# Optimization experiments

Hardware: AMD Instinct MI355X
Metric: run time of the kernel (lower is better)

## Reference

```python
import jax, jax.numpy as jnp
import numpy as np

SR = 44100        # sample rate (init kwarg)
WINDOWS = 2048    # fft window size (init kwarg)
B, P = 128, 192   # batch, number of peaking filters


def setup_inputs() -> dict:
    key = jax.random.key(0)
    k1, k2, k3 = jax.random.split(key, 3)
    # center frequencies in (40 Hz, 0.45*sr), gains in dB, quality factors in [0.5, 2)
    center = jax.random.uniform(k1, (B, P), minval=40.0, maxval=0.45 * SR, dtype=jnp.float32)
    gain = 6.0 * jax.random.normal(k2, (B, P), dtype=jnp.float32)
    q = jax.random.uniform(k3, (B, P), minval=0.5, maxval=2.0, dtype=jnp.float32)
    return {"center": center, "gain": gain, "q": q}


def _biquad(a, b, windows):
    # a, b: [..., 3] filter taps; rfft zero-pads to `windows` samples.
    iir = jnp.fft.rfft(a, n=windows, axis=-1)  # [..., windows//2+1] complex
    fir = jnp.fft.rfft(b, n=windows, axis=-1)
    return fir / iir


def reference(center, gain, q):
    """Peaking equalizer: [..., windows//2+1] complex frequency response."""
    w0 = (2.0 * np.pi / SR) * center
    A = jnp.exp(gain * (np.log(10.0) / 40.0))
    alpha = jnp.sin(w0) / 2.0 / q
    cos_w0 = jnp.cos(w0)
    b0 = 1.0 + alpha * A
    b1 = -2.0 * cos_w0
    b2 = 1.0 - alpha * A
    a0 = 1.0 + alpha / A
    a1 = -2.0 * cos_w0
    a2 = 1.0 - alpha / A
    return _biquad(jnp.stack([a0, a1, a2], axis=-1),
                   jnp.stack([b0, b1, b2], axis=-1), WINDOWS)
```

## Files before the change

### kernel.cpp

```cpp
#include <hip/hip_runtime.h>
#include <math.h>

constexpr int NBINS = 1025;
constexpr int NROWS = 128 * 192;
constexpr int RPB   = 16;
constexpr int NBLK  = NROWS / RPB;

__device__ inline unsigned int pack_bf16(float im, float re) {
    unsigned int u;
    asm("v_cvt_pk_bf16_f32 %0, %1, %2" : "=v"(u) : "v"(im), "v"(re));
    return u;
}

__global__ __launch_bounds__(256) void eq_kernel(
    const float* __restrict__ center,
    const float* __restrict__ gain,
    const float* __restrict__ q,
    unsigned int* __restrict__ out)
{
    __shared__ float2 tab[NBINS];
    __shared__ float4 rp[RPB];

    const int tid  = threadIdx.x;
    const int wave = tid >> 6;
    const int lane = tid & 63;

    if (tid < RPB) {
        const int row = blockIdx.x * RPB + tid;
        float w0 = 1.4247585730565955e-4f * center[row];
        float sh, ch;
        sincosf(0.5f * w0, &sh, &ch);
        float A = exp2f(0.08304820237218406f * gain[row]);
        float alpha = sh * ch / q[row];
        float g2 = alpha / A;
        float gd = alpha * A - g2;
        rp[tid] = make_float4(sh, 0.25f * alpha * alpha, 0.25f * g2 * g2, 0.5f * gd);
    }
    for (int k = tid; k < NBINS; k += 256) {
        float st, ct;
        sincosf((float)k * 1.5339807878856412e-3f, &st, &ct);
        tab[k] = make_float2(st, 2.0f * st * ct);
    }
    __syncthreads();

    for (int j = 0; j < 4; ++j) {
        const int r   = wave * 4 + j;
        const int row = blockIdx.x * RPB + r;
        const float4 P = rp[r];
        const int koff = row & 1;
        unsigned int* __restrict__ orow = out + (size_t)row * NBINS;
        uint2* __restrict__ op = (uint2*)(orow + koff);
        if (lane == 0)
            orow[koff ? 0 : 1024] = 0x3F800000u;
        #pragma unroll
        for (int i = 0; i < 8; ++i) {
            const int k = koff + 2 * lane + (i << 7);
            const float2 t0 = tab[k];
            const float2 t1 = tab[k + 1];
            float dp0 = (P.x - t0.x) * (P.x + t0.x);
            float dp1 = (P.x - t1.x) * (P.x + t1.x);
            float D20 = dp0 * dp0,  D21 = dp1 * dp1;
            float S20 = t0.y * t0.y, S21 = t1.y * t1.y;
            float i0 = __builtin_amdgcn_rcpf(fmaf(P.z, S20, D20));
            float i1 = __builtin_amdgcn_rcpf(fmaf(P.z, S21, D21));
            float re0 = fmaf(P.y, S20, D20) * i0;
            float re1 = fmaf(P.y, S21, D21) * i1;
            float im0 = P.w * t0.y * dp0 * i0;
            float im1 = P.w * t1.y * dp1 * i1;
            op[lane + (i << 6)] = make_uint2(pack_bf16(im0, re0),
                                             pack_bf16(im1, re1));
        }
    }
}

extern "C" void kernel_launch(void* const* d_in, const int* in_sizes, int n_in,
                              void* d_out, int out_size, void* d_ws, size_t ws_size,
                              hipStream_t stream) {
    const float* center = (const float*)d_in[0];
    const float* gain   = (const float*)d_in[1];
    const float* q      = (const float*)d_in[2];
    eq_kernel<<<NBLK, 256, 0, stream>>>(center, gain, q, (unsigned int*)d_out);
}
```

Baseline: 109.9 us.

## Write output as flat 16-byte stores across block rows with swizzled LDS table

Treats the block's 16 output rows as one contiguous buffer and has each thread emit a 16-byte store of four bins, replacing per-row 8-byte stores and the special-case scalar write at row edges. The sin table in LDS is XOR-swizzled to avoid bank conflicts from the new access stride. This widens global stores and removes the per-row alignment handling, at the cost of boundary branches that straddle row ends and index arithmetic per iteration.

```diff
diff --git a/kernel.cpp b/kernel.cpp
--- a/kernel.cpp
+++ b/kernel.cpp
@@ -5,12 +5,15 @@
 constexpr int NROWS = 128 * 192;
 constexpr int RPB   = 16;
 constexpr int NBLK  = NROWS / RPB;
+constexpr int STPB  = RPB * NBINS / 4;
 
 __device__ inline unsigned int pack_bf16(float im, float re) {
     unsigned int u;
     asm("v_cvt_pk_bf16_f32 %0, %1, %2" : "=v"(u) : "v"(im), "v"(re));
     return u;
 }
+
+__device__ inline int swz(int b) { return b ^ ((b >> 4) & 0x18); }
 
 __global__ __launch_bounds__(256) void eq_kernel(
     const float* __restrict__ center,
@@ -22,11 +25,10 @@
     __shared__ float4 rp[RPB];
 
     const int tid  = threadIdx.x;
-    const int wave = tid >> 6;
-    const int lane = tid & 63;
+    const int row0 = blockIdx.x * RPB;
 
     if (tid < RPB) {
-        const int row = blockIdx.x * RPB + tid;
+        const int row = row0 + tid;
         float w0 = 1.4247585730565955e-4f * center[row];
         float sh, ch;
         sincosf(0.5f * w0, &sh, &ch);
@@ -36,40 +38,48 @@
         float gd = alpha * A - g2;
         rp[tid] = make_float4(sh, 0.25f * alpha * alpha, 0.25f * g2 * g2, 0.5f * gd);
     }
+    char* tb = (char*)tab;
     for (int k = tid; k < NBINS; k += 256) {
         float st, ct;
         sincosf((float)k * 1.5339807878856412e-3f, &st, &ct);
-        tab[k] = make_float2(st, 2.0f * st * ct);
+        *(float2*)(tb + swz(8 * k)) = make_float2(st, 2.0f * st * ct);
     }
     __syncthreads();
 
-    for (int j = 0; j < 4; ++j) {
-        const int r   = wave * 4 + j;
-        const int row = blockIdx.x * RPB + r;
-        const float4 P = rp[r];
-        const int koff = row & 1;
-        unsigned int* __restrict__ orow = out + (size_t)row * NBINS;
-        uint2* __restrict__ op = (uint2*)(orow + koff);
-        if (lane == 0)
-            orow[koff ? 0 : 1024] = 0x3F800000u;
-        #pragma unroll
-        for (int i = 0; i < 8; ++i) {
-            const int k = koff + 2 * lane + (i << 7);
-            const float2 t0 = tab[k];
-            const float2 t1 = tab[k + 1];
-            float dp0 = (P.x - t0.x) * (P.x + t0.x);
-            float dp1 = (P.x - t1.x) * (P.x + t1.x);
-            float D20 = dp0 * dp0,  D21 = dp1 * dp1;
-            float S20 = t0.y * t0.y, S21 = t1.y * t1.y;
-            float i0 = __builtin_amdgcn_rcpf(fmaf(P.z, S20, D20));
-            float i1 = __builtin_amdgcn_rcpf(fmaf(P.z, S21, D21));
-            float re0 = fmaf(P.y, S20, D20) * i0;
-            float re1 = fmaf(P.y, S21, D21) * i1;
-            float im0 = P.w * t0.y * dp0 * i0;
-            float im1 = P.w * t1.y * dp1 * i1;
-            op[lane + (i << 6)] = make_uint2(pack_bf16(im0, re0),
-                                             pack_bf16(im1, re1));
+    uint4* __restrict__ ob = (uint4*)(out + (size_t)row0 * NBINS);
+    int k = 4 * tid;
+    int r = 0;
+    for (int si = tid; si < STPB; si += 256) {
+        uint4 res;
+        unsigned int* rw = (unsigned int*)&res;
+        if (k <= NBINS - 4) {
+            const float4 P = rp[r];
+            #pragma unroll
+            for (int j = 0; j < 4; ++j) {
+                const float2 t = *(const float2*)(tb + swz(8 * (k + j)));
+                float dp = (P.x - t.x) * (P.x + t.x);
+                float D2 = dp * dp, S2 = t.y * t.y;
+                float inv = __builtin_amdgcn_rcpf(fmaf(P.z, S2, D2));
+                rw[j] = pack_bf16(P.w * t.y * dp * inv,
+                                  fmaf(P.y, S2, D2) * inv);
+            }
+        } else {
+            #pragma unroll
+            for (int j = 0; j < 4; ++j) {
+                int kj = k + j, rj = r;
+                if (kj >= NBINS) { kj -= NBINS; ++rj; }
+                const float4 P = rp[rj];
+                const float2 t = *(const float2*)(tb + swz(8 * kj));
+                float dp = (P.x - t.x) * (P.x + t.x);
+                float D2 = dp * dp, S2 = t.y * t.y;
+                float inv = __builtin_amdgcn_rcpf(fmaf(P.z, S2, D2));
+                rw[j] = pack_bf16(P.w * t.y * dp * inv,
+                                  fmaf(P.y, S2, D2) * inv);
+            }
         }
+        ob[si] = res;
+        k += 1024;
+        if (k >= NBINS) { k -= NBINS; ++r; }
     }
 }
 
```

Result: slower. 114.3 us (+3.9%).
